# Kernel optimization log

Measured on AMD Instinct MI355X. Metric: run time of the kernel, lower is better.

## Reference

```python
import jax, jax.numpy as jnp
import numpy as np

EPS_ATTN = 1e-6
EPS_LN = 1e-5
NHEAD = 8


def _layernorm(x, g, b):
    mu = jnp.mean(x, axis=-1, keepdims=True)
    var = jnp.mean(jnp.square(x - mu), axis=-1, keepdims=True)
    return (x - mu) * jax.lax.rsqrt(var + EPS_LN) * g + b


def _feature_map(x):
    return jax.nn.elu(x) + 1.0


def setup_inputs() -> dict:
    key = jax.random.key(0)
    ks = jax.random.split(key, 8)
    N, L, S, C = 4, 8192, 8192, 256
    s = 1.0 / np.sqrt(C)
    return {
        "x": jax.random.normal(ks[0], (N, L, C), jnp.float32),
        "source": jax.random.normal(ks[1], (N, S, C), jnp.float32),
        "Wq": jax.random.normal(ks[2], (C, C), jnp.float32) * s,
        "Wk": jax.random.normal(ks[3], (C, C), jnp.float32) * s,
        "Wv": jax.random.normal(ks[4], (C, C), jnp.float32) * s,
        "Wmerge": jax.random.normal(ks[5], (C, C), jnp.float32) * s,
        "W1": jax.random.normal(ks[6], (2 * C, 2 * C), jnp.float32) * s,
        "W2": jax.random.normal(ks[7], (2 * C, C), jnp.float32) * s,
        "g1": jnp.ones((C,), jnp.float32),
        "b1": jnp.zeros((C,), jnp.float32),
        "g2": jnp.ones((C,), jnp.float32),
        "b2": jnp.zeros((C,), jnp.float32),
    }


def reference(x, source, Wq, Wk, Wv, Wmerge, W1, W2, g1, b1, g2, b2):
    N, L, C = x.shape
    S = source.shape[1]
    h, d = NHEAD, C // NHEAD

    q = (x @ Wq).reshape(N, L, h, d)
    k = (source @ Wk).reshape(N, S, h, d)
    v = (source @ Wv).reshape(N, S, h, d)

    Q = _feature_map(q)          # [N,L,h,d]
    K = _feature_map(k)          # [N,S,h,d]
    Vn = v / S                   # values / v_length

    KV = jnp.einsum('nshd,nshv->nhdv', K, Vn)             # [N,h,d,d]
    Ksum = K.sum(axis=1)                                  # [N,h,d]
    Z = 1.0 / (jnp.einsum('nlhd,nhd->nlh', Q, Ksum) + EPS_ATTN)
    msg = jnp.einsum('nlhd,nhdv,nlh->nlhv', Q, KV, Z) * S  # [N,L,h,d]

    msg = msg.reshape(N, L, C) @ Wmerge
    msg = _layernorm(msg, g1, b1)
    hcat = jnp.concatenate([x, msg], axis=2)              # [N,L,2C]
    msg = jax.nn.relu(hcat @ W1) @ W2
    msg = _layernorm(msg, g2, b2)
    return x + msg
```

## Files before the change

### kernel.cpp

```cpp
#include <hip/hip_runtime.h>
#include <hip/hip_bf16.h>
#include <stdint.h>

typedef __hip_bfloat16 bf16;
typedef __attribute__((ext_vector_type(8))) short short8;
typedef __attribute__((ext_vector_type(4))) short bf16x4;
typedef __attribute__((ext_vector_type(4))) float f32x4;

#define EPS_ATTN 1e-6f
#define EPS_LN   1e-5f

__device__ __forceinline__ float b2f(short s) {
    return __builtin_bit_cast(float, (unsigned)((unsigned short)s) << 16);
}
__device__ __forceinline__ short f2b(float f) {
    return __builtin_bit_cast(short, __float2bfloat16(f));
}

__device__ __forceinline__ void async16(const void* g, void* l) {
    __builtin_amdgcn_global_load_lds(
        (const __attribute__((address_space(1))) void*)g,
        (__attribute__((address_space(3))) void*)l,
        16, 0, 0);
}

__global__ __launch_bounds__(256)
void k_prep(const float* __restrict__ x, const float* __restrict__ src,
            bf16* __restrict__ x_bf, bf16* __restrict__ s_bf,
            const float* __restrict__ Wq, const float* __restrict__ Wk,
            const float* __restrict__ Wv, const float* __restrict__ Wm,
            const float* __restrict__ W1, const float* __restrict__ W2,
            bf16* __restrict__ WqT, bf16* __restrict__ WkT,
            bf16* __restrict__ WvT, bf16* __restrict__ WmT,
            bf16* __restrict__ W1T, bf16* __restrict__ W2T)
{
    __shared__ float tile[64][65];
    const int blk = blockIdx.x;
    if (blk < 8192) {
        const float* in = (blk < 4096) ? x : src;
        bf16* out       = (blk < 4096) ? x_bf : s_bf;
        const long id = (long)(blk & 4095) * 256 + threadIdx.x;
        const float4 a = ((const float4*)in)[id * 2];
        const float4 b = ((const float4*)in)[id * 2 + 1];
        short8 o;
        o[0] = f2b(a.x); o[1] = f2b(a.y); o[2] = f2b(a.z); o[3] = f2b(a.w);
        o[4] = f2b(b.x); o[5] = f2b(b.y); o[6] = f2b(b.z); o[7] = f2b(b.w);
        ((short8*)out)[id] = o;
        return;
    }
    const int b = blk - 8192;
    const float* W; bf16* WT; int K, N, local;
    if      (b < 16)  { W = Wq; WT = WqT; K = 256; N = 256; local = b; }
    else if (b < 32)  { W = Wk; WT = WkT; K = 256; N = 256; local = b - 16; }
    else if (b < 48)  { W = Wv; WT = WvT; K = 256; N = 256; local = b - 32; }
    else if (b < 64)  { W = Wm; WT = WmT; K = 256; N = 256; local = b - 48; }
    else if (b < 128) { W = W1; WT = W1T; K = 512; N = 512; local = b - 64; }
    else              { W = W2; WT = W2T; K = 512; N = 256; local = b - 128; }
    const int tk = K / 64;
    const int k0 = (local % tk) * 64, n0 = (local / tk) * 64;
    const int ty = threadIdx.x >> 4, tx = threadIdx.x & 15;
    #pragma unroll
    for (int i = 0; i < 4; ++i) {
        const int k = ty + i * 16;
        const float4 v = *(const float4*)&W[(long)(k0 + k) * N + n0 + tx * 4];
        tile[k][tx * 4 + 0] = v.x; tile[k][tx * 4 + 1] = v.y;
        tile[k][tx * 4 + 2] = v.z; tile[k][tx * 4 + 3] = v.w;
    }
    __syncthreads();
    #pragma unroll
    for (int i = 0; i < 4; ++i) {
        const int n = ty + i * 16;
        bf16x4 o;
        #pragma unroll
        for (int j = 0; j < 4; ++j) o[j] = f2b(tile[tx * 4 + j][n]);
        *(bf16x4*)&WT[(long)(n0 + n) * K + k0 + tx * 4] = o;
    }
}

__global__ __launch_bounds__(512)
void k_kvproj(const bf16* __restrict__ A, const bf16* __restrict__ BT,
              bf16* __restrict__ partKV, float* __restrict__ partKs,
              float escale)
{
    __shared__ __attribute__((aligned(16))) bf16 S[32768];
    bf16* Asm = S;
    bf16* Bsm = S + 8192;
    bf16* KT  = S;
    bf16* VT  = S + 16384;

    const int t = threadIdx.x, w = t >> 6, lane = t & 63;
    const int wm = w >> 2, wn = w & 3;
    const int flat = blockIdx.y * gridDim.x + blockIdx.x;
    const int swz  = (flat & 7) * 64 + (flat >> 3);
    const int cid  = swz >> 1;
    const int hh   = swz & 1;
    const long row0 = (long)cid * 128;
    const int lr = lane >> 3, lc = (lane & 7) * 8;
    const int lg = lane >> 4, l15 = lane & 15;

    f32x4 acc[4][4] = {};

    for (int kt = 0; kt < 256; kt += 64) {
        #pragma unroll
        for (int i = 0; i < 2; ++i) {
            const int g = w * 2 + i;
            async16(A + (row0 + g * 8 + lr) * 256 + kt + lc, &Asm[g * 512]);
        }
        #pragma unroll
        for (int i = 0; i < 4; ++i) {
            const int g = w * 4 + i;
            const long brow = (g < 16)
                ? (long)(hh * 128 + g * 8 + lr)
                : (long)(256 + hh * 128 + (g - 16) * 8 + lr);
            async16(BT + brow * 256 + kt + lc, &Bsm[g * 512]);
        }
        __syncthreads();
        #pragma unroll
        for (int ks = 0; ks < 2; ++ks) {
            short8 a[4], b[4];
            #pragma unroll
            for (int m = 0; m < 4; ++m)
                a[m] = *(const short8*)&Asm[(wm*64 + m*16 + l15)*64 + ks*32 + lg*8];
            #pragma unroll
            for (int n = 0; n < 4; ++n)
                b[n] = *(const short8*)&Bsm[(wn*64 + n*16 + l15)*64 + ks*32 + lg*8];
            #pragma unroll
            for (int m = 0; m < 4; ++m)
                #pragma unroll
                for (int n = 0; n < 4; ++n)
                    acc[m][n] = __builtin_amdgcn_mfma_f32_16x16x32_bf16(a[m], b[n], acc[m][n], 0, 0, 0);
        }
        __syncthreads();
    }

    const bool isK = wn < 2;
    bf16* tile = isK ? KT : VT;
    #pragma unroll
    for (int m = 0; m < 4; ++m) {
        #pragma unroll
        for (int n = 0; n < 4; ++n) {
            #pragma unroll
            for (int r = 0; r < 4; ++r) {
                const int row = wm * 64 + m * 16 + lg * 4 + r;
                const int col = (wn & 1) * 64 + n * 16 + l15;
                float v = acc[m][n][r];
                if (isK) v = v > 0.f ? v + 1.f : __expf(v);
                else     v *= escale;
                tile[row * 128 + col] = __float2bfloat16(v);
            }
        }
    }
    __syncthreads();

    const int h_l = t >> 7;
    const int d   = (t & 127) >> 2;
    const int vg  = t & 3;
    float a2[8] = {};
    float ks = 0.f;
    #pragma unroll 4
    for (int row = 0; row < 128; ++row) {
        const float kd = __bfloat162float(KT[row * 128 + h_l * 32 + d]);
        ks += kd;
        const short8 vv = *(const short8*)&VT[row * 128 + h_l * 32 + vg * 8];
        #pragma unroll
        for (int u = 0; u < 8; ++u) a2[u] += kd * b2f(vv[u]);
    }
    short8 o;
    #pragma unroll
    for (int u = 0; u < 8; ++u) o[u] = f2b(a2[u]);
    *(short8*)&partKV[(long)cid * 8192 + (hh * 4 + h_l) * 1024 + d * 32 + vg * 8] = o;
    if (vg == 0) partKs[cid * 256 + (hh * 4 + h_l) * 32 + d] = ks;
}

__global__ __launch_bounds__(256)
void k_kvred1(const bf16* __restrict__ partKV, const float* __restrict__ partKs,
              bf16* __restrict__ part2, float* __restrict__ part2Ks)
{
    const int bid = blockIdx.x;
    const int c8 = bid & 7, h = (bid >> 3) & 7, n = bid >> 6;
    const int t = threadIdx.x;
    const int d = t >> 3, vg = t & 7;
    float s[4] = {};
    #pragma unroll
    for (int j = 0; j < 8; ++j) {
        const int cid = n * 64 + c8 * 8 + j;
        const bf16x4 p = *(const bf16x4*)&partKV[(long)cid * 8192 + h * 1024 + d * 32 + vg * 4];
        #pragma unroll
        for (int jj = 0; jj < 4; ++jj) s[jj] += b2f(p[jj]);
    }
    bf16x4 o;
    #pragma unroll
    for (int jj = 0; jj < 4; ++jj) o[jj] = f2b(s[jj]);
    *(bf16x4*)&part2[(long)(c8 * 4 + n) * 8192 + h * 1024 + d * 32 + vg * 4] = o;
    if (vg == 0) {
        float ks = 0.f;
        #pragma unroll
        for (int j = 0; j < 8; ++j) {
            const int cid = n * 64 + c8 * 8 + j;
            ks += partKs[cid * 256 + h * 32 + d];
        }
        part2Ks[(c8 * 4 + n) * 256 + h * 32 + d] = ks;
    }
}

__global__ __launch_bounds__(256)
void k_kvred2(const bf16* __restrict__ part2, const float* __restrict__ part2Ks,
              bf16* __restrict__ KVb)
{
    const int b = blockIdx.x;
    const int n = b >> 3, h = b & 7;
    const int t = threadIdx.x;
    const int d = t >> 3, vg = t & 7;
    float s[4] = {};
    #pragma unroll
    for (int c8 = 0; c8 < 8; ++c8) {
        const bf16x4 p = *(const bf16x4*)&part2[(long)(c8 * 4 + n) * 8192 + h * 1024 + d * 32 + vg * 4];
        #pragma unroll
        for (int j = 0; j < 4; ++j) s[j] += b2f(p[j]);
    }
    bf16* dst = KVb + ((long)n * 8 + h) * 1536 + d * 48;
    bf16x4 o;
    #pragma unroll
    for (int j = 0; j < 4; ++j) o[j] = f2b(s[j]);
    *(bf16x4*)&dst[vg * 4] = o;
    if (vg == 0) {
        float ks = 0.f;
        #pragma unroll
        for (int c8 = 0; c8 < 8; ++c8) ks += part2Ks[(c8 * 4 + n) * 256 + h * 32 + d];
        short8 z0 = {};
        z0[0] = f2b(ks);
        *(short8*)&dst[32] = z0;
        short8 zz = {};
        *(short8*)&dst[40] = zz;
    }
}

__global__ __launch_bounds__(512)
void k_qaml(const bf16* __restrict__ xb, const bf16* __restrict__ WqT,
            const bf16* __restrict__ WmT, const bf16* __restrict__ KVb,
            const float* __restrict__ g, const float* __restrict__ b,
            bf16* __restrict__ msgln)
{
    __shared__ __attribute__((aligned(16))) bf16 Asm[64 * 64];
    __shared__ __attribute__((aligned(16))) bf16 Bsm[256 * 64];
    __shared__ __attribute__((aligned(16))) bf16 QM[64 * 264];
    __shared__ float lnS[4][64];
    __shared__ float lnQ[4][64];
    const int t = threadIdx.x, w = t >> 6, lane = t & 63;
    const int wm = w >> 2, wn = w & 3;
    const long row0 = (long)blockIdx.x * 64;
    const int n_b = (int)(row0 >> 13);
    const int lr = lane >> 3, lc = (lane & 7) * 8;
    const int lg = lane >> 4, l15 = lane & 15;

    {
        f32x4 acc[2][4] = {};
        for (int kt = 0; kt < 256; kt += 64) {
            async16(xb + (row0 + w * 8 + lr) * 256 + kt + lc, &Asm[w * 512]);
            #pragma unroll
            for (int i = 0; i < 4; ++i) {
                const int ch = i * 8 + w;
                async16(WqT + (long)(ch * 8 + lr) * 256 + kt + lc, &Bsm[ch * 512]);
            }
            __syncthreads();
            #pragma unroll
            for (int ks = 0; ks < 2; ++ks) {
                short8 a[2], bb[4];
                #pragma unroll
                for (int m = 0; m < 2; ++m)
                    a[m] = *(const short8*)&Asm[(wm*32 + m*16 + l15)*64 + ks*32 + lg*8];
                #pragma unroll
                for (int n = 0; n < 4; ++n)
                    bb[n] = *(const short8*)&Bsm[(wn*64 + n*16 + l15)*64 + ks*32 + lg*8];
                #pragma unroll
                for (int m = 0; m < 2; ++m)
                    #pragma unroll
                    for (int n = 0; n < 4; ++n)
                        acc[m][n] = __builtin_amdgcn_mfma_f32_16x16x32_bf16(a[m], bb[n], acc[m][n], 0, 0, 0);
            }
            __syncthreads();
        }
        #pragma unroll
        for (int m = 0; m < 2; ++m) {
            #pragma unroll
            for (int n = 0; n < 4; ++n) {
                #pragma unroll
                for (int r = 0; r < 4; ++r) {
                    const int row = wm * 32 + m * 16 + lg * 4 + r;
                    const int col = wn * 64 + n * 16 + l15;
                    float v = acc[m][n][r];
                    v = v > 0.f ? v + 1.f : __expf(v);
                    QM[row * 264 + col] = __float2bfloat16(v);
                }
            }
        }
    }
    __syncthreads();

    {
        const bf16* kvh = KVb + (long)n_b * 12288 + w * 1536;
        short8 b0, b1, bz;
        #pragma unroll
        for (int j = 0; j < 8; ++j) {
            const int drow = (lg * 8 + j) * 48;
            b0[j] = __builtin_bit_cast(short, kvh[drow + l15]);
            b1[j] = __builtin_bit_cast(short, kvh[drow + 16 + l15]);
            bz[j] = __builtin_bit_cast(short, kvh[drow + 32 + l15]);
        }
        f32x4 ra0[4], ra1[4];
        #pragma unroll
        for (int m2 = 0; m2 < 4; ++m2) {
            const short8 a = *(const short8*)&QM[(m2 * 16 + l15) * 264 + w * 32 + lg * 8];
            f32x4 a0 = {}, a1 = {}, az = {};
            a0 = __builtin_amdgcn_mfma_f32_16x16x32_bf16(a, b0, a0, 0, 0, 0);
            a1 = __builtin_amdgcn_mfma_f32_16x16x32_bf16(a, b1, a1, 0, 0, 0);
            az = __builtin_amdgcn_mfma_f32_16x16x32_bf16(a, bz, az, 0, 0, 0);
            #pragma unroll
            for (int r = 0; r < 4; ++r) {
                const float z   = __shfl(az[r], lane & 48);
                const float inv = 8192.f / (z + EPS_ATTN);
                ra0[m2][r] = a0[r] * inv;
                ra1[m2][r] = a1[r] * inv;
            }
        }
        __syncthreads();
        #pragma unroll
        for (int m2 = 0; m2 < 4; ++m2) {
            #pragma unroll
            for (int r = 0; r < 4; ++r) {
                const int row = m2 * 16 + lg * 4 + r;
                QM[row * 264 + w * 32 + l15]      = __float2bfloat16(ra0[m2][r]);
                QM[row * 264 + w * 32 + 16 + l15] = __float2bfloat16(ra1[m2][r]);
            }
        }
    }
    __syncthreads();

    f32x4 acc[2][4] = {};
    for (int kt = 0; kt < 256; kt += 64) {
        #pragma unroll
        for (int i = 0; i < 4; ++i) {
            const int ch = i * 8 + w;
            async16(WmT + (long)(ch * 8 + lr) * 256 + kt + lc, &Bsm[ch * 512]);
        }
        __syncthreads();
        #pragma unroll
        for (int ks = 0; ks < 2; ++ks) {
            short8 a[2], bb[4];
            #pragma unroll
            for (int m = 0; m < 2; ++m)
                a[m] = *(const short8*)&QM[(wm*32 + m*16 + l15) * 264 + kt + ks*32 + lg*8];
            #pragma unroll
            for (int n = 0; n < 4; ++n)
                bb[n] = *(const short8*)&Bsm[(wn*64 + n*16 + l15)*64 + ks*32 + lg*8];
            #pragma unroll
            for (int m = 0; m < 2; ++m)
                #pragma unroll
                for (int n = 0; n < 4; ++n)
                    acc[m][n] = __builtin_amdgcn_mfma_f32_16x16x32_bf16(a[m], bb[n], acc[m][n], 0, 0, 0);
        }
        __syncthreads();
    }

    #pragma unroll
    for (int m = 0; m < 2; ++m) {
        #pragma unroll
        for (int r = 0; r < 4; ++r) {
            float ls = 0.f, lq = 0.f;
            #pragma unroll
            for (int n = 0; n < 4; ++n) {
                const float v = acc[m][n][r];
                ls += v; lq += v * v;
            }
            #pragma unroll
            for (int o = 1; o < 16; o <<= 1) {
                ls += __shfl_xor(ls, o);
                lq += __shfl_xor(lq, o);
            }
            if (l15 == 0) {
                const int row = wm * 32 + m * 16 + lg * 4 + r;
                lnS[wn][row] = ls;
                lnQ[wn][row] = lq;
            }
        }
    }
    __syncthreads();

    float gv[4], bv[4];
    #pragma unroll
    for (int n = 0; n < 4; ++n) {
        const int col = wn * 64 + n * 16 + l15;
        gv[n] = g[col]; bv[n] = b[col];
    }
    #pragma unroll
    for (int m = 0; m < 2; ++m) {
        #pragma unroll
        for (int r = 0; r < 4; ++r) {
            const int row = wm * 32 + m * 16 + lg * 4 + r;
            const float S  = lnS[0][row] + lnS[1][row] + lnS[2][row] + lnS[3][row];
            const float Qq = lnQ[0][row] + lnQ[1][row] + lnQ[2][row] + lnQ[3][row];
            const float mean = S * (1.f / 256.f);
            const float var  = Qq * (1.f / 256.f) - mean * mean;
            const float rstd = rsqrtf(var + EPS_LN);
            const long grow = row0 + row;
            #pragma unroll
            for (int n = 0; n < 4; ++n) {
                const int col = wn * 64 + n * 16 + l15;
                const float y = (acc[m][n][r] - mean) * rstd * gv[n] + bv[n];
                msgln[grow * 256 + col] = __float2bfloat16(y);
            }
        }
    }
}

__global__ __launch_bounds__(512, 2)
void k_gemmW1_8p(const bf16* __restrict__ A0, const bf16* __restrict__ A1,
                 const bf16* __restrict__ BT, bf16* __restrict__ C)
{
    __shared__ __attribute__((aligned(16))) bf16 S[65536];
    const int t = threadIdx.x, w = t >> 6, lane = t & 63;
    const int wm = w >> 2, wn = w & 3;
    const int lg = lane >> 4, l15 = lane & 15;
    const int orig = blockIdx.y * gridDim.x + blockIdx.x;
    const int swz  = (orig & 7) * 32 + (orig >> 3);
    const long row0 = (long)(swz >> 1) * 256;
    const long col0 = (long)(swz & 1) * 256;

    f32x4 acc[8][4] = {};
    short8 av[4], bv0[4], bv1[4];

    auto stageA = [&](int tile, int half) {
        if (tile >= 8) return;
        const bf16* Asrc = (tile < 4) ? A0 : A1;
        const int kbase = (tile & 3) * 64;
        #pragma unroll
        for (int i = 0; i < 2; ++i) {
            const int cbase = i * 512 + w * 64;
            const int c = cbase + lane;
            const int srow = c >> 3;
            const int lcol = 8 * ((c & 7) ^ (srow & 7));
            async16(Asrc + (row0 + half * 128 + srow) * 256 + kbase + lcol,
                    &S[(tile & 1) * 32768 + half * 8192 + cbase * 8]);
        }
    };
    auto stageB = [&](int tile, int half) {
        if (tile >= 8) return;
        const int kbase = tile * 64;
        #pragma unroll
        for (int i = 0; i < 2; ++i) {
            const int cbase = i * 512 + w * 64;
            const int c = cbase + lane;
            const int srow = c >> 3;
            const int lcol = 8 * ((c & 7) ^ (srow & 7));
            async16(BT + (col0 + half * 128 + srow) * 512 + kbase + lcol,
                    &S[(tile & 1) * 32768 + 16384 + half * 8192 + cbase * 8]);
        }
    };

#define RD_A(BUF, MH, KS) do { _Pragma("unroll")                               \
    for (int m_ = 0; m_ < 4; ++m_) {                                           \
        const int row_ = wm * 128 + (MH) * 64 + m_ * 16 + l15;                 \
        av[m_] = *(const short8*)&S[(BUF) * 32768 + row_ * 64 +                \
                 (((KS) * 32 + lg * 8) ^ ((row_ & 7) << 3))]; } } while (0)

#define RD_B(BUF, KS, BV) do { _Pragma("unroll")                               \
    for (int n_ = 0; n_ < 4; ++n_) {                                           \
        const int row_ = wn * 64 + n_ * 16 + l15;                              \
        (BV)[n_] = *(const short8*)&S[(BUF) * 32768 + 16384 + row_ * 64 +      \
                 (((KS) * 32 + lg * 8) ^ ((row_ & 7) << 3))]; } } while (0)

#define DO_MFMA(MH, BV) do { __builtin_amdgcn_s_setprio(1); _Pragma("unroll")  \
    for (int m_ = 0; m_ < 4; ++m_) { _Pragma("unroll")                         \
        for (int n_ = 0; n_ < 4; ++n_)                                         \
            acc[(MH) * 4 + m_][n_] = __builtin_amdgcn_mfma_f32_16x16x32_bf16(  \
                av[m_], (BV)[n_], acc[(MH) * 4 + m_][n_], 0, 0, 0); }          \
    __builtin_amdgcn_s_setprio(0); } while (0)

#define BAR() __builtin_amdgcn_s_barrier()

    stageB(0, 0); stageB(0, 1); stageA(0, 0); stageA(0, 1);
    stageB(1, 0); stageB(1, 1);
    asm volatile("s_waitcnt vmcnt(4)" ::: "memory");
    BAR();

    for (int it = 0; it < 4; ++it) {
        const int T1 = 2 * it + 1;
        RD_B(0, 0, bv0); RD_A(0, 0, 0); stageA(T1, 0);
        BAR(); DO_MFMA(0, bv0); BAR();
        RD_B(0, 1, bv1); RD_A(0, 0, 1); stageA(T1, 1);
        BAR(); DO_MFMA(0, bv1); BAR();
        RD_A(0, 1, 0); stageB(T1 + 1, 0);
        BAR(); DO_MFMA(1, bv0); BAR();
        RD_A(0, 1, 1); stageB(T1 + 1, 1);
        BAR(); DO_MFMA(1, bv1);
        if (it == 3) asm volatile("s_waitcnt vmcnt(0)" ::: "memory");
        else         asm volatile("s_waitcnt vmcnt(4)" ::: "memory");
        BAR();
        RD_B(1, 0, bv0); RD_A(1, 0, 0); stageA(T1 + 1, 0);
        BAR(); DO_MFMA(0, bv0); BAR();
        RD_B(1, 1, bv1); RD_A(1, 0, 1); stageA(T1 + 1, 1);
        BAR(); DO_MFMA(0, bv1); BAR();
        RD_A(1, 1, 0); stageB(T1 + 2, 0);
        BAR(); DO_MFMA(1, bv0); BAR();
        RD_A(1, 1, 1); stageB(T1 + 2, 1);
        BAR(); DO_MFMA(1, bv1);
        if (it < 3) asm volatile("s_waitcnt vmcnt(4)" ::: "memory");
        BAR();
    }

    #pragma unroll
    for (int mi = 0; mi < 8; ++mi) {
        #pragma unroll
        for (int n = 0; n < 4; ++n) {
            #pragma unroll
            for (int r = 0; r < 4; ++r) {
                const long row = row0 + wm * 128 + mi * 16 + lg * 4 + r;
                const long col = col0 + wn * 64 + n * 16 + l15;
                const float v = acc[mi][n][r];
                C[row * 512 + col] = __float2bfloat16(v > 0.f ? v : 0.f);
            }
        }
    }
#undef RD_A
#undef RD_B
#undef DO_MFMA
#undef BAR
}

__global__ __launch_bounds__(512, 2)
void k_ln2_8p(const bf16* __restrict__ A, const bf16* __restrict__ BT,
              const float* __restrict__ g, const float* __restrict__ b,
              const float* __restrict__ xres, float* __restrict__ out)
{
    __shared__ __attribute__((aligned(16))) bf16 S[65536];
    const int t = threadIdx.x, w = t >> 6, lane = t & 63;
    const int wm = w >> 2, wn = w & 3;
    const int lg = lane >> 4, l15 = lane & 15;
    const int orig = blockIdx.x;
    const int swz  = (orig & 7) * 16 + (orig >> 3);
    const long row0 = (long)swz * 256;

    f32x4 acc[8][4] = {};
    short8 av[4], bv0[4], bv1[4];

    auto stageA = [&](int tile, int half) {
        if (tile >= 8) return;
        const int kbase = tile * 64;
        #pragma unroll
        for (int i = 0; i < 2; ++i) {
            const int cbase = i * 512 + w * 64;
            const int c = cbase + lane;
            const int srow = c >> 3;
            const int lcol = 8 * ((c & 7) ^ (srow & 7));
            async16(A + (row0 + half * 128 + srow) * 512 + kbase + lcol,
                    &S[(tile & 1) * 32768 + half * 8192 + cbase * 8]);
        }
    };
    auto stageB = [&](int tile, int half) {
        if (tile >= 8) return;
        const int kbase = tile * 64;
        #pragma unroll
        for (int i = 0; i < 2; ++i) {
            const int cbase = i * 512 + w * 64;
            const int c = cbase + lane;
            const int srow = c >> 3;
            const int lcol = 8 * ((c & 7) ^ (srow & 7));
            async16(BT + (long)(half * 128 + srow) * 512 + kbase + lcol,
                    &S[(tile & 1) * 32768 + 16384 + half * 8192 + cbase * 8]);
        }
    };

#define RD_A(BUF, MH, KS) do { _Pragma("unroll")                               \
    for (int m_ = 0; m_ < 4; ++m_) {                                           \
        const int row_ = wm * 128 + (MH) * 64 + m_ * 16 + l15;                 \
        av[m_] = *(const short8*)&S[(BUF) * 32768 + row_ * 64 +                \
                 (((KS) * 32 + lg * 8) ^ ((row_ & 7) << 3))]; } } while (0)

#define RD_B(BUF, KS, BV) do { _Pragma("unroll")                               \
    for (int n_ = 0; n_ < 4; ++n_) {                                           \
        const int row_ = wn * 64 + n_ * 16 + l15;                              \
        (BV)[n_] = *(const short8*)&S[(BUF) * 32768 + 16384 + row_ * 64 +      \
                 (((KS) * 32 + lg * 8) ^ ((row_ & 7) << 3))]; } } while (0)

#define DO_MFMA(MH, BV) do { __builtin_amdgcn_s_setprio(1); _Pragma("unroll")  \
    for (int m_ = 0; m_ < 4; ++m_) { _Pragma("unroll")                         \
        for (int n_ = 0; n_ < 4; ++n_)                                         \
            acc[(MH) * 4 + m_][n_] = __builtin_amdgcn_mfma_f32_16x16x32_bf16(  \
                av[m_], (BV)[n_], acc[(MH) * 4 + m_][n_], 0, 0, 0); }          \
    __builtin_amdgcn_s_setprio(0); } while (0)

#define BAR() __builtin_amdgcn_s_barrier()

    stageB(0, 0); stageB(0, 1); stageA(0, 0); stageA(0, 1);
    stageB(1, 0); stageB(1, 1);
    asm volatile("s_waitcnt vmcnt(4)" ::: "memory");
    BAR();

    for (int it = 0; it < 4; ++it) {
        const int T1 = 2 * it + 1;
        RD_B(0, 0, bv0); RD_A(0, 0, 0); stageA(T1, 0);
        BAR(); DO_MFMA(0, bv0); BAR();
        RD_B(0, 1, bv1); RD_A(0, 0, 1); stageA(T1, 1);
        BAR(); DO_MFMA(0, bv1); BAR();
        RD_A(0, 1, 0); stageB(T1 + 1, 0);
        BAR(); DO_MFMA(1, bv0); BAR();
        RD_A(0, 1, 1); stageB(T1 + 1, 1);
        BAR(); DO_MFMA(1, bv1);
        if (it == 3) asm volatile("s_waitcnt vmcnt(0)" ::: "memory");
        else         asm volatile("s_waitcnt vmcnt(4)" ::: "memory");
        BAR();
        RD_B(1, 0, bv0); RD_A(1, 0, 0); stageA(T1 + 1, 0);
        BAR(); DO_MFMA(0, bv0); BAR();
        RD_B(1, 1, bv1); RD_A(1, 0, 1); stageA(T1 + 1, 1);
        BAR(); DO_MFMA(0, bv1); BAR();
        RD_A(1, 1, 0); stageB(T1 + 2, 0);
        BAR(); DO_MFMA(1, bv0); BAR();
        RD_A(1, 1, 1); stageB(T1 + 2, 1);
        BAR(); DO_MFMA(1, bv1);
        if (it < 3) asm volatile("s_waitcnt vmcnt(4)" ::: "memory");
        BAR();
    }

    __syncthreads();
    float* lnS = (float*)S;
    float* lnQ = (float*)((char*)S + 4096);

    #pragma unroll
    for (int mi = 0; mi < 8; ++mi) {
        #pragma unroll
        for (int r = 0; r < 4; ++r) {
            float ls = 0.f, lq = 0.f;
            #pragma unroll
            for (int n = 0; n < 4; ++n) {
                const float v = acc[mi][n][r];
                ls += v; lq += v * v;
            }
            #pragma unroll
            for (int o = 1; o < 16; o <<= 1) {
                ls += __shfl_xor(ls, o);
                lq += __shfl_xor(lq, o);
            }
            if (l15 == 0) {
                const int row = wm * 128 + mi * 16 + lg * 4 + r;
                lnS[wn * 256 + row] = ls;
                lnQ[wn * 256 + row] = lq;
            }
        }
    }
    __syncthreads();

    float gv[4], bv[4];
    #pragma unroll
    for (int n = 0; n < 4; ++n) {
        const int col = wn * 64 + n * 16 + l15;
        gv[n] = g[col]; bv[n] = b[col];
    }
    #pragma unroll
    for (int mi = 0; mi < 8; ++mi) {
        #pragma unroll
        for (int r = 0; r < 4; ++r) {
            const int row = wm * 128 + mi * 16 + lg * 4 + r;
            const float Sm = lnS[row] + lnS[256 + row] + lnS[512 + row] + lnS[768 + row];
            const float Qq = lnQ[row] + lnQ[256 + row] + lnQ[512 + row] + lnQ[768 + row];
            const float mean = Sm * (1.f / 256.f);
            const float var  = Qq * (1.f / 256.f) - mean * mean;
            const float rstd = rsqrtf(var + EPS_LN);
            const long grow = row0 + row;
            #pragma unroll
            for (int n = 0; n < 4; ++n) {
                const int col = wn * 64 + n * 16 + l15;
                const float y = (acc[mi][n][r] - mean) * rstd * gv[n] + bv[n];
                out[grow * 256 + col] = xres[grow * 256 + col] + y;
            }
        }
    }
#undef RD_A
#undef RD_B
#undef DO_MFMA
#undef BAR
}

extern "C" void kernel_launch(void* const* d_in, const int* in_sizes, int n_in,
                              void* d_out, int out_size, void* d_ws, size_t ws_size,
                              hipStream_t stream)
{
    const float* x      = (const float*)d_in[0];
    const float* source = (const float*)d_in[1];
    const float* Wq     = (const float*)d_in[2];
    const float* Wk     = (const float*)d_in[3];
    const float* Wv     = (const float*)d_in[4];
    const float* Wm     = (const float*)d_in[5];
    const float* W1     = (const float*)d_in[6];
    const float* W2     = (const float*)d_in[7];
    const float* g1     = (const float*)d_in[8];
    const float* b1     = (const float*)d_in[9];
    const float* g2     = (const float*)d_in[10];
    const float* b2     = (const float*)d_in[11];
    float* out = (float*)d_out;

    const size_t U = 32768ull * 256ull;
    char* w = (char*)d_ws;

    bf16* x_bf  = (bf16*)(w + 0 * U * 2);
    bf16* s_bf  = (bf16*)(w + 1 * U * 2);
    bf16* msgln = (bf16*)(w + 2 * U * 2);
    bf16* t_bf  = (bf16*)(w + 3 * U * 2);

    char* wx = w + 7 * U * 2;
    bf16* WqT = (bf16*)wx; wx += 65536 * 2;
    bf16* WkT = (bf16*)wx; wx += 65536 * 2;
    bf16* WvT = (bf16*)wx; wx += 65536 * 2;
    bf16* WmT = (bf16*)wx; wx += 65536 * 2;
    bf16* W1T = (bf16*)wx; wx += 262144 * 2;
    bf16* W2T = (bf16*)wx; wx += 131072 * 2;
    bf16* partKV = (bf16*)wx; wx += 2097152 * 2;
    float* partKs = (float*)wx; wx += 65536 * 4;
    bf16* part2  = (bf16*)wx; wx += 262144 * 2;
    float* part2Ks = (float*)wx; wx += 8192 * 4;
    bf16* KVb    = (bf16*)wx; wx += 49152 * 2;

    const dim3 blk(256);

    k_prep<<<8352, blk, 0, stream>>>(x, source, x_bf, s_bf,
                                     Wq, Wk, Wv, Wm, W1, W2,
                                     WqT, WkT, WvT, WmT, W1T, W2T);

    k_kvproj<<<dim3(256, 2), dim3(512), 0, stream>>>(s_bf, WkT, partKV, partKs,
                                                     1.f / 8192.f);

    k_kvred1<<<256, blk, 0, stream>>>(partKV, partKs, part2, part2Ks);
    k_kvred2<<<32, blk, 0, stream>>>(part2, part2Ks, KVb);

    k_qaml<<<512, dim3(512), 0, stream>>>(x_bf, WqT, WmT, KVb, g1, b1, msgln);

    k_gemmW1_8p<<<dim3(128, 2), dim3(512), 0, stream>>>(x_bf, msgln, W1T, t_bf);
    k_ln2_8p<<<128, dim3(512), 0, stream>>>(t_bf, W2T, g2, b2, x, out);
}
```

Measured before the change: 131.3 us.

## Triple-buffer qaml GEMM loads with async prefetch and merge KV reduction kernels

Rewrites the two GEMM phases in k_qaml (x·Wq and attn·Wmerge) to use a three-stage LDS ring with async global-to-LDS prefetch. Explicit vmcnt waits and raw s_barriers replace full __syncthreads, and the Wmerge tiles are prefetched while the attention step runs. This aims to hide global load latency behind MFMA work. It also folds the two-level KV partial reduction into a single 32-block kernel, removing one launch and the intermediate buffer at the cost of less parallelism in the reduction. LDS use grows substantially, which may reduce occupancy, and the hand-counted vmcnt values must match the number of issued loads exactly.

```diff
diff --git a/kernel.cpp b/kernel.cpp
--- a/kernel.cpp
+++ b/kernel.cpp
@@ -173,48 +173,18 @@
 }
 
 __global__ __launch_bounds__(256)
-void k_kvred1(const bf16* __restrict__ partKV, const float* __restrict__ partKs,
-              bf16* __restrict__ part2, float* __restrict__ part2Ks)
+void k_kvred(const bf16* __restrict__ partKV, const float* __restrict__ partKs,
+             bf16* __restrict__ KVb)
 {
-    const int bid = blockIdx.x;
-    const int c8 = bid & 7, h = (bid >> 3) & 7, n = bid >> 6;
+    const int bk = blockIdx.x;
+    const int n = bk >> 3, h = bk & 7;
     const int t = threadIdx.x;
     const int d = t >> 3, vg = t & 7;
     float s[4] = {};
-    #pragma unroll
-    for (int j = 0; j < 8; ++j) {
-        const int cid = n * 64 + c8 * 8 + j;
+    #pragma unroll 8
+    for (int i = 0; i < 64; ++i) {
+        const int cid = n * 64 + i;
         const bf16x4 p = *(const bf16x4*)&partKV[(long)cid * 8192 + h * 1024 + d * 32 + vg * 4];
-        #pragma unroll
-        for (int jj = 0; jj < 4; ++jj) s[jj] += b2f(p[jj]);
-    }
-    bf16x4 o;
-    #pragma unroll
-    for (int jj = 0; jj < 4; ++jj) o[jj] = f2b(s[jj]);
-    *(bf16x4*)&part2[(long)(c8 * 4 + n) * 8192 + h * 1024 + d * 32 + vg * 4] = o;
-    if (vg == 0) {
-        float ks = 0.f;
-        #pragma unroll
-        for (int j = 0; j < 8; ++j) {
-            const int cid = n * 64 + c8 * 8 + j;
-            ks += partKs[cid * 256 + h * 32 + d];
-        }
-        part2Ks[(c8 * 4 + n) * 256 + h * 32 + d] = ks;
-    }
-}
-
-__global__ __launch_bounds__(256)
-void k_kvred2(const bf16* __restrict__ part2, const float* __restrict__ part2Ks,
-              bf16* __restrict__ KVb)
-{
-    const int b = blockIdx.x;
-    const int n = b >> 3, h = b & 7;
-    const int t = threadIdx.x;
-    const int d = t >> 3, vg = t & 7;
-    float s[4] = {};
-    #pragma unroll
-    for (int c8 = 0; c8 < 8; ++c8) {
-        const bf16x4 p = *(const bf16x4*)&part2[(long)(c8 * 4 + n) * 8192 + h * 1024 + d * 32 + vg * 4];
         #pragma unroll
         for (int j = 0; j < 4; ++j) s[j] += b2f(p[j]);
     }
@@ -225,8 +195,11 @@
     *(bf16x4*)&dst[vg * 4] = o;
     if (vg == 0) {
         float ks = 0.f;
-        #pragma unroll
-        for (int c8 = 0; c8 < 8; ++c8) ks += part2Ks[(c8 * 4 + n) * 256 + h * 32 + d];
+        #pragma unroll 8
+        for (int i = 0; i < 64; ++i) {
+            const int cid = n * 64 + i;
+            ks += partKs[cid * 256 + h * 32 + d];
+        }
         short8 z0 = {};
         z0[0] = f2b(ks);
         *(short8*)&dst[32] = z0;
@@ -241,8 +214,8 @@
             const float* __restrict__ g, const float* __restrict__ b,
             bf16* __restrict__ msgln)
 {
-    __shared__ __attribute__((aligned(16))) bf16 Asm[64 * 64];
-    __shared__ __attribute__((aligned(16))) bf16 Bsm[256 * 64];
+    __shared__ __attribute__((aligned(16))) bf16 A3[3][4096];
+    __shared__ __attribute__((aligned(16))) bf16 B3[3][16384];
     __shared__ __attribute__((aligned(16))) bf16 QM[64 * 264];
     __shared__ float lnS[4][64];
     __shared__ float lnQ[4][64];
@@ -253,68 +226,95 @@
     const int lr = lane >> 3, lc = (lane & 7) * 8;
     const int lg = lane >> 4, l15 = lane & 15;
 
-    {
-        f32x4 acc[2][4] = {};
-        for (int kt = 0; kt < 256; kt += 64) {
-            async16(xb + (row0 + w * 8 + lr) * 256 + kt + lc, &Asm[w * 512]);
-            #pragma unroll
-            for (int i = 0; i < 4; ++i) {
-                const int ch = i * 8 + w;
-                async16(WqT + (long)(ch * 8 + lr) * 256 + kt + lc, &Bsm[ch * 512]);
-            }
-            __syncthreads();
-            #pragma unroll
-            for (int ks = 0; ks < 2; ++ks) {
-                short8 a[2], bb[4];
-                #pragma unroll
-                for (int m = 0; m < 2; ++m)
-                    a[m] = *(const short8*)&Asm[(wm*32 + m*16 + l15)*64 + ks*32 + lg*8];
+    auto stage1 = [&](int kti, int buf) {
+        const int kt = kti * 64;
+        async16(xb + (row0 + w * 8 + lr) * 256 + kt + lc, &A3[buf][w * 512]);
+        #pragma unroll
+        for (int i = 0; i < 4; ++i) {
+            const int ch = i * 8 + w;
+            async16(WqT + (long)(ch * 8 + lr) * 256 + kt + lc, &B3[buf][ch * 512]);
+        }
+    };
+    auto stage2 = [&](int kti, int buf) {
+        const int kt = kti * 64;
+        #pragma unroll
+        for (int i = 0; i < 4; ++i) {
+            const int ch = i * 8 + w;
+            async16(WmT + (long)(ch * 8 + lr) * 256 + kt + lc, &B3[buf][ch * 512]);
+        }
+    };
+
+    f32x4 acc1[2][4] = {};
+    stage1(0, 0); stage1(1, 1);
+    asm volatile("s_waitcnt vmcnt(5)" ::: "memory");
+    __builtin_amdgcn_s_barrier();
+
+    #pragma unroll
+    for (int tt = 0; tt < 4; ++tt) {
+        const int buf = tt % 3;
+        short8 a[2][2], bb[2][4];
+        #pragma unroll
+        for (int ks = 0; ks < 2; ++ks) {
+            #pragma unroll
+            for (int m = 0; m < 2; ++m)
+                a[ks][m] = *(const short8*)&A3[buf][(wm*32 + m*16 + l15)*64 + ks*32 + lg*8];
+            #pragma unroll
+            for (int n = 0; n < 4; ++n)
+                bb[ks][n] = *(const short8*)&B3[buf][(wn*64 + n*16 + l15)*64 + ks*32 + lg*8];
+        }
+        if (tt < 2) stage1(tt + 2, (tt + 2) % 3);
+        #pragma unroll
+        for (int ks = 0; ks < 2; ++ks)
+            #pragma unroll
+            for (int m = 0; m < 2; ++m)
                 #pragma unroll
                 for (int n = 0; n < 4; ++n)
-                    bb[n] = *(const short8*)&Bsm[(wn*64 + n*16 + l15)*64 + ks*32 + lg*8];
-                #pragma unroll
-                for (int m = 0; m < 2; ++m)
-                    #pragma unroll
-                    for (int n = 0; n < 4; ++n)
-                        acc[m][n] = __builtin_amdgcn_mfma_f32_16x16x32_bf16(a[m], bb[n], acc[m][n], 0, 0, 0);
-            }
-            __syncthreads();
-        }
-        #pragma unroll
-        for (int m = 0; m < 2; ++m) {
-            #pragma unroll
-            for (int n = 0; n < 4; ++n) {
-                #pragma unroll
-                for (int r = 0; r < 4; ++r) {
-                    const int row = wm * 32 + m * 16 + lg * 4 + r;
-                    const int col = wn * 64 + n * 16 + l15;
-                    float v = acc[m][n][r];
-                    v = v > 0.f ? v + 1.f : __expf(v);
-                    QM[row * 264 + col] = __float2bfloat16(v);
-                }
-            }
-        }
-    }
-    __syncthreads();
+                    acc1[m][n] = __builtin_amdgcn_mfma_f32_16x16x32_bf16(a[ks][m], bb[ks][n], acc1[m][n], 0, 0, 0);
+        if (tt < 2)       asm volatile("s_waitcnt vmcnt(5)" ::: "memory");
+        else if (tt == 2) asm volatile("s_waitcnt vmcnt(0)" ::: "memory");
+        __builtin_amdgcn_s_barrier();
+    }
+
+    #pragma unroll
+    for (int m = 0; m < 2; ++m) {
+        #pragma unroll
+        for (int n = 0; n < 4; ++n) {
+            #pragma unroll
+            for (int r = 0; r < 4; ++r) {
+                const int row = wm * 32 + m * 16 + lg * 4 + r;
+                const int col = wn * 64 + n * 16 + l15;
+                float v = acc1[m][n][r];
+                v = v > 0.f ? v + 1.f : __expf(v);
+                QM[row * 264 + col] = __float2bfloat16(v);
+            }
+        }
+    }
+
+    const bf16* kvh = KVb + (long)n_b * 12288 + w * 1536;
+    short8 kb0, kb1, kbz;
+    #pragma unroll
+    for (int j = 0; j < 8; ++j) {
+        const int drow = (lg * 8 + j) * 48;
+        kb0[j] = __builtin_bit_cast(short, kvh[drow + l15]);
+        kb1[j] = __builtin_bit_cast(short, kvh[drow + 16 + l15]);
+        kbz[j] = __builtin_bit_cast(short, kvh[drow + 32 + l15]);
+    }
+
+    stage2(0, 1); stage2(1, 2);
+
+    asm volatile("s_waitcnt lgkmcnt(0)" ::: "memory");
+    __builtin_amdgcn_sched_barrier(0);
+    __builtin_amdgcn_s_barrier();
 
     {
-        const bf16* kvh = KVb + (long)n_b * 12288 + w * 1536;
-        short8 b0, b1, bz;
-        #pragma unroll
-        for (int j = 0; j < 8; ++j) {
-            const int drow = (lg * 8 + j) * 48;
-            b0[j] = __builtin_bit_cast(short, kvh[drow + l15]);
-            b1[j] = __builtin_bit_cast(short, kvh[drow + 16 + l15]);
-            bz[j] = __builtin_bit_cast(short, kvh[drow + 32 + l15]);
-        }
         f32x4 ra0[4], ra1[4];
         #pragma unroll
         for (int m2 = 0; m2 < 4; ++m2) {
             const short8 a = *(const short8*)&QM[(m2 * 16 + l15) * 264 + w * 32 + lg * 8];
             f32x4 a0 = {}, a1 = {}, az = {};
-            a0 = __builtin_amdgcn_mfma_f32_16x16x32_bf16(a, b0, a0, 0, 0, 0);
-            a1 = __builtin_amdgcn_mfma_f32_16x16x32_bf16(a, b1, a1, 0, 0, 0);
-            az = __builtin_amdgcn_mfma_f32_16x16x32_bf16(a, bz, az, 0, 0, 0);
+            a0 = __builtin_amdgcn_mfma_f32_16x16x32_bf16(a, kb0, a0, 0, 0, 0);
+            a1 = __builtin_amdgcn_mfma_f32_16x16x32_bf16(a, kb1, a1, 0, 0, 0);
+            az = __builtin_amdgcn_mfma_f32_16x16x32_bf16(a, kbz, az, 0, 0, 0);
             #pragma unroll
             for (int r = 0; r < 4; ++r) {
                 const float z   = __shfl(az[r], lane & 48);
@@ -323,7 +323,9 @@
                 ra1[m2][r] = a1[r] * inv;
             }
         }
-        __syncthreads();
+        asm volatile("s_waitcnt lgkmcnt(0)" ::: "memory");
+        __builtin_amdgcn_sched_barrier(0);
+        __builtin_amdgcn_s_barrier();
         #pragma unroll
         for (int m2 = 0; m2 < 4; ++m2) {
             #pragma unroll
@@ -334,32 +336,38 @@
             }
         }
     }
-    __syncthreads();
-
-    f32x4 acc[2][4] = {};
-    for (int kt = 0; kt < 256; kt += 64) {
-        #pragma unroll
-        for (int i = 0; i < 4; ++i) {
-            const int ch = i * 8 + w;
-            async16(WmT + (long)(ch * 8 + lr) * 256 + kt + lc, &Bsm[ch * 512]);
-        }
-        __syncthreads();
+    asm volatile("s_waitcnt lgkmcnt(0)" ::: "memory");
+    __builtin_amdgcn_sched_barrier(0);
+    __builtin_amdgcn_s_barrier();
+
+    asm volatile("s_waitcnt vmcnt(4)" ::: "memory");
+    __builtin_amdgcn_s_barrier();
+
+    f32x4 acc2[2][4] = {};
+    #pragma unroll
+    for (int tt = 0; tt < 4; ++tt) {
+        const int buf = (tt + 1) % 3;
+        short8 a[2][2], bb[2][4];
         #pragma unroll
         for (int ks = 0; ks < 2; ++ks) {
-            short8 a[2], bb[4];
             #pragma unroll
             for (int m = 0; m < 2; ++m)
-                a[m] = *(const short8*)&QM[(wm*32 + m*16 + l15) * 264 + kt + ks*32 + lg*8];
+                a[ks][m] = *(const short8*)&QM[(wm*32 + m*16 + l15) * 264 + tt*64 + ks*32 + lg*8];
             #pragma unroll
             for (int n = 0; n < 4; ++n)
-                bb[n] = *(const short8*)&Bsm[(wn*64 + n*16 + l15)*64 + ks*32 + lg*8];
+                bb[ks][n] = *(const short8*)&B3[buf][(wn*64 + n*16 + l15)*64 + ks*32 + lg*8];
+        }
+        if (tt < 2) stage2(tt + 2, (tt + 3) % 3);
+        #pragma unroll
+        for (int ks = 0; ks < 2; ++ks)
             #pragma unroll
             for (int m = 0; m < 2; ++m)
                 #pragma unroll
                 for (int n = 0; n < 4; ++n)
-                    acc[m][n] = __builtin_amdgcn_mfma_f32_16x16x32_bf16(a[m], bb[n], acc[m][n], 0, 0, 0);
-        }
-        __syncthreads();
+                    acc2[m][n] = __builtin_amdgcn_mfma_f32_16x16x32_bf16(a[ks][m], bb[ks][n], acc2[m][n], 0, 0, 0);
+        if (tt < 2)       asm volatile("s_waitcnt vmcnt(4)" ::: "memory");
+        else if (tt == 2) asm volatile("s_waitcnt vmcnt(0)" ::: "memory");
+        __builtin_amdgcn_s_barrier();
     }
 
     #pragma unroll
@@ -369,7 +377,7 @@
             float ls = 0.f, lq = 0.f;
             #pragma unroll
             for (int n = 0; n < 4; ++n) {
-                const float v = acc[m][n][r];
+                const float v = acc2[m][n][r];
                 ls += v; lq += v * v;
             }
             #pragma unroll
@@ -406,7 +414,7 @@
             #pragma unroll
             for (int n = 0; n < 4; ++n) {
                 const int col = wn * 64 + n * 16 + l15;
-                const float y = (acc[m][n][r] - mean) * rstd * gv[n] + bv[n];
+                const float y = (acc2[m][n][r] - mean) * rstd * gv[n] + bv[n];
                 msgln[grow * 256 + col] = __float2bfloat16(y);
             }
         }
@@ -715,8 +723,6 @@
     bf16* W2T = (bf16*)wx; wx += 131072 * 2;
     bf16* partKV = (bf16*)wx; wx += 2097152 * 2;
     float* partKs = (float*)wx; wx += 65536 * 4;
-    bf16* part2  = (bf16*)wx; wx += 262144 * 2;
-    float* part2Ks = (float*)wx; wx += 8192 * 4;
     bf16* KVb    = (bf16*)wx; wx += 49152 * 2;
 
     const dim3 blk(256);
@@ -728,8 +734,7 @@
     k_kvproj<<<dim3(256, 2), dim3(512), 0, stream>>>(s_bf, WkT, partKV, partKs,
                                                      1.f / 8192.f);
 
-    k_kvred1<<<256, blk, 0, stream>>>(partKV, partKs, part2, part2Ks);
-    k_kvred2<<<32, blk, 0, stream>>>(part2, part2Ks, KVb);
+    k_kvred<<<32, blk, 0, stream>>>(partKV, partKs, KVb);
 
     k_qaml<<<512, dim3(512), 0, stream>>>(x_bf, WqT, WmT, KVb, g1, b1, msgln);
 
```

After: 136.7 us. 4.1% more time.
